# Performance work log

Measured on AMD Instinct MI355X. Metric: run time of the kernel, lower is better.

Reference implementation:

```python
import jax, jax.numpy as jnp
import numpy as np

B, T, D = 4, 2048, 2048
H = 16
NOPE, ROPE, VD = 64, 64, 128
QK = NOPE + ROPE  # 128
KV_R, Q_R = 512, 1024
EPS = 1e-6
THETA = 10000.0
SCALE = 1.0 / np.sqrt(QK)


def rmsnorm(x, g):
    var = jnp.mean(jnp.square(x), axis=-1, keepdims=True)
    return x * jax.lax.rsqrt(var + EPS) * g


def rope_tables(seq_len, dim):
    inv_freq = 1.0 / (THETA ** (np.arange(0, dim, 2, dtype=np.float32) / dim))
    t = np.arange(seq_len, dtype=np.float32)
    freqs = np.outer(t, inv_freq)              # [T, dim/2]
    emb = np.concatenate([freqs, freqs], -1)   # [T, dim]
    return jnp.asarray(np.cos(emb)), jnp.asarray(np.sin(emb))


def rotate_half(x):
    x1, x2 = jnp.split(x, 2, axis=-1)
    return jnp.concatenate([-x2, x1], axis=-1)


def apply_rope(x, cos, sin):
    # x: [B,H,S,dim]; cos/sin: [S,dim] -> broadcast over B,H
    return x * cos[None, None] + rotate_half(x) * sin[None, None]


def setup_inputs() -> dict:
    key = jax.random.key(0)
    ks = jax.random.split(key, 10)
    w = lambda k, shp: jax.random.normal(k, shp, jnp.float32) * 0.02
    return {
        'x': jax.random.normal(ks[0], (B, T, D), jnp.float32),
        'w_q_down': w(ks[1], (D, Q_R)),
        'g_q_down': jnp.ones((Q_R,), jnp.float32),
        'w_q_up': w(ks[2], (Q_R, H * QK)),
        'w_kv_down': w(ks[3], (D, KV_R)),
        'g_kv_down': jnp.ones((KV_R,), jnp.float32),
        'w_k_up': w(ks[4], (KV_R, H * NOPE)),
        'w_v_up': w(ks[5], (KV_R, H * VD)),
        'w_k_rope': w(ks[6], (D, ROPE)),
        'g_q': jnp.ones((QK,), jnp.float32),
        'g_k': jnp.ones((QK,), jnp.float32),
        'w_gate': w(ks[7], (D, H * VD)),
        'w_o': w(ks[8], (H * VD, D)),
    }


def reference(x, w_q_down, g_q_down, w_q_up, w_kv_down, g_kv_down,
              w_k_up, w_v_up, w_k_rope, g_q, g_k, w_gate, w_o):
    cos, sin = rope_tables(T, ROPE)

    # Low-rank Q: down-proj -> RMSNorm -> up-proj
    q_c = rmsnorm(x @ w_q_down, g_q_down)                       # [B,T,Q_R]
    q = (q_c @ w_q_up).reshape(B, T, H, QK).transpose(0, 2, 1, 3)  # [B,H,T,QK]
    q_nope, q_rope = q[..., :NOPE], q[..., NOPE:]

    # Low-rank KV compression
    c_kv = rmsnorm(x @ w_kv_down, g_kv_down)                    # [B,S,KV_R]
    k_rope = x @ w_k_rope                                       # [B,S,ROPE]
    S = T
    k_nope = (c_kv @ w_k_up).reshape(B, S, H, NOPE).transpose(0, 2, 1, 3)
    v = (c_kv @ w_v_up).reshape(B, S, H, VD).transpose(0, 2, 1, 3)

    # Decoupled RoPE: shared k_rope broadcast over heads
    k_rope = jnp.broadcast_to(k_rope[:, None], (B, H, S, ROPE))
    q_rope = apply_rope(q_rope, cos[:T], sin[:T])
    k_rope = apply_rope(k_rope, cos[:S], sin[:S])

    q = rmsnorm(jnp.concatenate([q_nope, q_rope], -1), g_q)     # [B,H,T,QK]
    k = rmsnorm(jnp.concatenate([k_nope, k_rope], -1), g_k)     # [B,H,S,QK]

    # Causal SDPA
    scores = jnp.einsum('bhtd,bhsd->bhts', q, k) * SCALE
    mask = jnp.tril(jnp.ones((T, S), bool))
    scores = jnp.where(mask, scores, jnp.finfo(scores.dtype).min)
    attn = jax.nn.softmax(scores, axis=-1)
    out = jnp.einsum('bhts,bhsd->bhtd', attn, v)                # [B,H,T,VD]

    # Gating
    gate = (x @ w_gate).reshape(B, T, H, VD).transpose(0, 2, 1, 3)
    out = out * jax.nn.silu(gate)

    out = out.transpose(0, 2, 1, 3).reshape(B, T, H * VD)
    return out @ w_o
```

## Files before the change

### kernel.cpp

```cpp
#include <hip/hip_runtime.h>
#include <hip/hip_bf16.h>
#include <math.h>

typedef __bf16 bf16_t;
typedef __bf16 bf16x4 __attribute__((ext_vector_type(4)));
typedef __bf16 bf16x8 __attribute__((ext_vector_type(8)));
typedef float f32x4 __attribute__((ext_vector_type(4)));

#define SCALE_F 0.08838834764831845f
#define SMAX_F 14.0f

#define GLOAD_LDS16(gp, lp)                                              \
    __builtin_amdgcn_global_load_lds(                                    \
        (const __attribute__((address_space(1))) void*)(gp),             \
        (__attribute__((address_space(3))) void*)(lp), 16, 0, 0)

__global__ void k_convert(const float* __restrict__ in, bf16_t* __restrict__ out, int n) {
    int i = (blockIdx.x * 256 + threadIdx.x) * 4;
    if (i >= n) return;
    float4 f = *(const float4*)(in + i);
    out[i + 0] = (bf16_t)f.x;
    out[i + 1] = (bf16_t)f.y;
    out[i + 2] = (bf16_t)f.z;
    out[i + 3] = (bf16_t)f.w;
}

__global__ void k_transpose(const float* __restrict__ w, bf16_t* __restrict__ wt, int K, int N) {
    __shared__ float tile[32][33];
    int n0 = blockIdx.x * 32, k0 = blockIdx.y * 32;
    int tx = threadIdx.x & 31, ty = threadIdx.x >> 5;
#pragma unroll
    for (int i = 0; i < 32; i += 8)
        tile[ty + i][tx] = w[(size_t)(k0 + ty + i) * N + (n0 + tx)];
    __syncthreads();
#pragma unroll
    for (int i = 0; i < 32; i += 8)
        wt[(size_t)(n0 + ty + i) * K + (k0 + tx)] = (bf16_t)tile[tx][ty + i];
}

__global__ void k_rope_tables(float* __restrict__ cosT, float* __restrict__ sinT) {
    int idx = blockIdx.x * 256 + threadIdx.x;
    int t = idx >> 6, i = idx & 63;
    float invf = powf(10000.f, -(float)(i & 31) / 32.f);
    float ang = (float)t * invf;
    float s, c;
    sincosf(ang, &s, &c);
    cosT[idx] = c;
    sinT[idx] = s;
}

__global__ void k_rmsnorm(bf16_t* __restrict__ x, const float* __restrict__ g, int C) {
    bf16_t* p = x + (size_t)blockIdx.x * C;
    float ss = 0.f;
    for (int i = threadIdx.x; i < C; i += 256) {
        float v = (float)p[i];
        ss += v * v;
    }
#pragma unroll
    for (int m = 32; m; m >>= 1) ss += __shfl_xor(ss, m);
    __shared__ float red[4];
    if ((threadIdx.x & 63) == 0) red[threadIdx.x >> 6] = ss;
    __syncthreads();
    float tot = red[0] + red[1] + red[2] + red[3];
    float scale = rsqrtf(tot / (float)C + 1e-6f);
    for (int i = threadIdx.x; i < C; i += 256)
        p[i] = (bf16_t)((float)p[i] * scale * g[i]);
}

template <int OUTF32>
__global__ __launch_bounds__(256) void k_gemm(const bf16_t* __restrict__ A,
                                              const bf16_t* __restrict__ Bt,
                                              void* __restrict__ Cp, int M, int N, int K,
                                              size_t sA, size_t sB, size_t sC) {
    __shared__ bf16_t As[2][128 * 32];
    __shared__ bf16_t Bs[2][128 * 32];
    A += (size_t)blockIdx.z * sA;
    Bt += (size_t)blockIdx.z * sB;
    const size_t coff = (size_t)blockIdx.z * sC;
    const int bm = blockIdx.y * 128, bn = blockIdx.x * 128;
    const int tid = threadIdx.x, lane = tid & 63, wv = tid >> 6;
    const int quad = lane >> 4, l16 = lane & 15;
    const int wm = (wv >> 1) * 64, wn = (wv & 1) * 64;
    f32x4 acc[4][4] = {};
    const int sr0 = wv * 32 + (lane >> 2);
    const int scc = (lane & 3) * 8;
    const int lo0 = (wv * 2) * 512, lo1 = (wv * 2 + 1) * 512;
    const bool bok0 = (bn + sr0) < N;
    const bool bok1 = (bn + sr0 + 16) < N;
    for (int k0 = 0; k0 < K; k0 += 64) {
        const bf16_t* gA = A + (size_t)(bm + sr0) * K + k0 + scc;
        const bf16_t* gB = Bt + (size_t)(bn + sr0) * K + k0 + scc;
        GLOAD_LDS16(gA, As[0] + lo0);
        GLOAD_LDS16(gA + (size_t)16 * K, As[0] + lo1);
        GLOAD_LDS16(gA + 32, As[1] + lo0);
        GLOAD_LDS16(gA + (size_t)16 * K + 32, As[1] + lo1);
        if (bok0) {
            GLOAD_LDS16(gB, Bs[0] + lo0);
            GLOAD_LDS16(gB + 32, Bs[1] + lo0);
        }
        if (bok1) {
            GLOAD_LDS16(gB + (size_t)16 * K, Bs[0] + lo1);
            GLOAD_LDS16(gB + (size_t)16 * K + 32, Bs[1] + lo1);
        }
        __syncthreads();
#pragma unroll
        for (int hf = 0; hf < 2; ++hf) {
            bf16x8 af[4], bfr[4];
#pragma unroll
            for (int mi = 0; mi < 4; ++mi)
                af[mi] = *(bf16x8*)(As[hf] + (wm + mi * 16 + l16) * 32 + quad * 8);
#pragma unroll
            for (int ni = 0; ni < 4; ++ni)
                bfr[ni] = *(bf16x8*)(Bs[hf] + (wn + ni * 16 + l16) * 32 + quad * 8);
#pragma unroll
            for (int mi = 0; mi < 4; ++mi)
#pragma unroll
                for (int ni = 0; ni < 4; ++ni)
                    acc[mi][ni] = __builtin_amdgcn_mfma_f32_16x16x32_bf16(af[mi], bfr[ni],
                                                                          acc[mi][ni], 0, 0, 0);
        }
        __syncthreads();
    }
#pragma unroll
    for (int mi = 0; mi < 4; ++mi)
#pragma unroll
        for (int ni = 0; ni < 4; ++ni)
#pragma unroll
            for (int r = 0; r < 4; ++r) {
                int row = bm + wm + mi * 16 + quad * 4 + r;
                int col = bn + wn + ni * 16 + l16;
                if (col < N) {
                    if constexpr (OUTF32)
                        ((float*)Cp)[coff + (size_t)row * N + col] = acc[mi][ni][r];
                    else
                        ((bf16_t*)Cp)[coff + (size_t)row * N + col] = (bf16_t)acc[mi][ni][r];
                }
            }
}

__global__ void k_build_q(bf16_t* __restrict__ q, const float* __restrict__ g,
                          const float* __restrict__ cosT, const float* __restrict__ sinT) {
    int wid = blockIdx.x * 4 + (threadIdx.x >> 6);
    int lane = threadIdx.x & 63;
    int row = wid >> 4, h = wid & 15;
    int t = row & 2047;
    bf16_t* p = q + (size_t)row * 2048 + h * 128;
    float x0 = (float)p[lane];
    float x1 = (float)p[64 + lane];
    float xp = (float)p[64 + (lane ^ 32)];
    float c = cosT[t * 64 + lane], s = sinT[t * 64 + lane];
    float rot = (lane < 32) ? -xp : xp;
    float y1 = x1 * c + rot * s;
    float ss = x0 * x0 + y1 * y1;
#pragma unroll
    for (int m = 32; m; m >>= 1) ss += __shfl_xor(ss, m);
    float scale = rsqrtf(ss / 128.f + 1e-6f);
    p[lane] = (bf16_t)(x0 * scale * g[lane]);
    p[64 + lane] = (bf16_t)(y1 * scale * g[64 + lane]);
}

__global__ void k_build_k(const bf16_t* __restrict__ knope, const bf16_t* __restrict__ krope,
                          bf16_t* __restrict__ kout, const float* __restrict__ g,
                          const float* __restrict__ cosT, const float* __restrict__ sinT) {
    int wid = blockIdx.x * 4 + (threadIdx.x >> 6);
    int lane = threadIdx.x & 63;
    int row = wid >> 4, h = wid & 15;
    int t = row & 2047;
    float x0 = (float)knope[(size_t)row * 1024 + h * 64 + lane];
    float x1 = (float)krope[(size_t)row * 64 + lane];
    float xp = (float)krope[(size_t)row * 64 + (lane ^ 32)];
    float c = cosT[t * 64 + lane], s = sinT[t * 64 + lane];
    float rot = (lane < 32) ? -xp : xp;
    float y1 = x1 * c + rot * s;
    float ss = x0 * x0 + y1 * y1;
#pragma unroll
    for (int m = 32; m; m >>= 1) ss += __shfl_xor(ss, m);
    float scale = rsqrtf(ss / 128.f + 1e-6f);
    bf16_t* p = kout + (size_t)row * 2048 + h * 128;
    p[lane] = (bf16_t)(x0 * scale * g[lane]);
    p[64 + lane] = (bf16_t)(y1 * scale * g[64 + lane]);
}

__global__ __launch_bounds__(512, 4) void k_attn(const bf16_t* __restrict__ q,
                                                 const bf16_t* __restrict__ k,
                                                 const bf16_t* __restrict__ vT,
                                                 const bf16_t* __restrict__ gate,
                                                 bf16_t* __restrict__ o) {
    __shared__ bf16_t Ks[64 * 136];
    __shared__ bf16_t Vt[128 * 72];
    __shared__ float lbuf[128];
    const int qb = (int)gridDim.x - 1 - (int)blockIdx.x;
    const int bh = blockIdx.y;
    const int b = bh >> 4, h = bh & 15;
    const int t0 = qb * 128;
    const int tid = threadIdx.x, lane = tid & 63, wv = tid >> 6;
    const int quad = lane >> 4, l16 = lane & 15;
    const int wrow = t0 + wv * 16;

    bf16x8 aq[4];
    {
        const bf16_t* qp = q + ((size_t)(b * 2048 + wrow + l16)) * 2048 + h * 128 + quad * 8;
#pragma unroll
        for (int kk = 0; kk < 4; ++kk) aq[kk] = *(const bf16x8*)(qp + kk * 32);
    }
    f32x4 oacc[8] = {};
    float l_lane = 0.f;

    const bf16_t* vbase = vT + ((size_t)b * 2048 + (size_t)h * 128) * 2048;
    const bf16_t* kbase = k + ((size_t)b * 2048) * 2048 + h * 128;

    const int krow = tid >> 4;
    const int kcol = (tid & 15) * 8;
    const int kds = krow * 136 + kcol;
    const int vrow = tid >> 3;
    const int vcol = (tid & 7) * 8;
    const int a8 = tid & 7;
    const int pb0 = (a8 >> 2) * 32 + (a8 & 1) * 16 + ((a8 >> 1) & 1) * 4;
    const int vds = vrow * 72 + pb0;

    const int nkb = 2 * qb + 2;
    bf16x8 kreg0, kreg1, vreg0, vreg1;
    {
        kreg0 = *(const bf16x8*)(kbase + (size_t)krow * 2048 + kcol);
        kreg1 = *(const bf16x8*)(kbase + (size_t)(krow + 32) * 2048 + kcol);
        vreg0 = *(const bf16x8*)(vbase + (size_t)vrow * 2048 + vcol);
        vreg1 = *(const bf16x8*)(vbase + (size_t)(vrow + 64) * 2048 + vcol);
    }
    for (int kb = 0; kb < nkb; ++kb) {
        const int s0 = kb * 64;
        __syncthreads();
        *(bf16x8*)(Ks + kds) = kreg0;
        *(bf16x8*)(Ks + kds + 32 * 136) = kreg1;
        {
            bf16x4 v0lo = __builtin_shufflevector(vreg0, vreg0, 0, 1, 2, 3);
            bf16x4 v0hi = __builtin_shufflevector(vreg0, vreg0, 4, 5, 6, 7);
            bf16x4 v1lo = __builtin_shufflevector(vreg1, vreg1, 0, 1, 2, 3);
            bf16x4 v1hi = __builtin_shufflevector(vreg1, vreg1, 4, 5, 6, 7);
            *(bf16x4*)(Vt + vds) = v0lo;
            *(bf16x4*)(Vt + vds + 8) = v0hi;
            *(bf16x4*)(Vt + vds + 64 * 72) = v1lo;
            *(bf16x4*)(Vt + vds + 64 * 72 + 8) = v1hi;
        }
        __syncthreads();
        if (kb + 1 < nkb) {
            const int sn = s0 + 64;
            kreg0 = *(const bf16x8*)(kbase + (size_t)(sn + krow) * 2048 + kcol);
            kreg1 = *(const bf16x8*)(kbase + (size_t)(sn + krow + 32) * 2048 + kcol);
            vreg0 = *(const bf16x8*)(vbase + (size_t)vrow * 2048 + sn + vcol);
            vreg1 = *(const bf16x8*)(vbase + (size_t)(vrow + 64) * 2048 + sn + vcol);
        }
        if (s0 > wrow + 15) continue;
        f32x4 sc[4] = {};
#pragma unroll
        for (int ni = 0; ni < 4; ++ni)
#pragma unroll
            for (int kk = 0; kk < 4; ++kk) {
                bf16x8 ak = *(bf16x8*)(Ks + (ni * 16 + l16) * 136 + kk * 32 + quad * 8);
                sc[ni] = __builtin_amdgcn_mfma_f32_16x16x32_bf16(ak, aq[kk], sc[ni], 0, 0, 0);
            }
        const int tq = wrow + l16;
#pragma unroll
        for (int ni = 0; ni < 4; ++ni) {
            const int sb = s0 + ni * 16 + quad * 4;
#pragma unroll
            for (int r2 = 0; r2 < 4; ++r2) {
                float pv = __expf(sc[ni][r2] * SCALE_F - SMAX_F);
                if (sb + r2 > tq) pv = 0.f;
                sc[ni][r2] = pv;
                l_lane += pv;
            }
        }
        bf16x8 pa0, pa1;
#pragma unroll
        for (int r2 = 0; r2 < 4; ++r2) {
            pa0[r2] = (bf16_t)sc[0][r2];
            pa0[4 + r2] = (bf16_t)sc[1][r2];
            pa1[r2] = (bf16_t)sc[2][r2];
            pa1[4 + r2] = (bf16_t)sc[3][r2];
        }
#pragma unroll
        for (int nd = 0; nd < 8; ++nd) {
            bf16x8 bv = *(bf16x8*)(Vt + (nd * 16 + l16) * 72 + quad * 8);
            oacc[nd] = __builtin_amdgcn_mfma_f32_16x16x32_bf16(pa0, bv, oacc[nd], 0, 0, 0);
        }
#pragma unroll
        for (int nd = 0; nd < 8; ++nd) {
            bf16x8 bv = *(bf16x8*)(Vt + (nd * 16 + l16) * 72 + 32 + quad * 8);
            oacc[nd] = __builtin_amdgcn_mfma_f32_16x16x32_bf16(pa1, bv, oacc[nd], 0, 0, 0);
        }
    }
    l_lane += __shfl_xor(l_lane, 16);
    l_lane += __shfl_xor(l_lane, 32);
    if (quad == 0) lbuf[wv * 16 + l16] = l_lane;
    float rl[4];
#pragma unroll
    for (int r2 = 0; r2 < 4; ++r2) rl[r2] = 1.f / lbuf[wv * 16 + quad * 4 + r2];
#pragma unroll
    for (int nd = 0; nd < 8; ++nd) {
        int d = nd * 16 + l16;
#pragma unroll
        for (int r2 = 0; r2 < 4; ++r2) {
            int trow = wrow + quad * 4 + r2;
            size_t gi = ((size_t)(b * 2048 + trow)) * 2048 + h * 128 + d;
            float gt = (float)gate[gi];
            float sg = gt / (1.f + __expf(-gt));
            o[gi] = (bf16_t)((oacc[nd][r2] * rl[r2]) * sg);
        }
    }
}

extern "C" void kernel_launch(void* const* d_in, const int* in_sizes, int n_in,
                              void* d_out, int out_size, void* d_ws, size_t ws_size,
                              hipStream_t stream) {
    const float* x         = (const float*)d_in[0];
    const float* w_q_down  = (const float*)d_in[1];
    const float* g_q_down  = (const float*)d_in[2];
    const float* w_q_up    = (const float*)d_in[3];
    const float* w_kv_down = (const float*)d_in[4];
    const float* g_kv_down = (const float*)d_in[5];
    const float* w_k_up    = (const float*)d_in[6];
    const float* w_v_up    = (const float*)d_in[7];
    const float* w_k_rope  = (const float*)d_in[8];
    const float* g_q       = (const float*)d_in[9];
    const float* g_k       = (const float*)d_in[10];
    const float* w_gate    = (const float*)d_in[11];
    const float* w_o       = (const float*)d_in[12];
    float* out = (float*)d_out;

    char* base = (char*)d_ws;
    size_t off = 0;
    auto alloc = [&](size_t bytes) -> void* {
        void* p = base + off;
        off = (off + bytes + 255) & ~(size_t)255;
        return p;
    };
    const size_t MT = 8192;
    bf16_t* xb     = (bf16_t*)alloc(MT * 2048 * 2);
    bf16_t* wqd_t  = (bf16_t*)alloc((size_t)1024 * 2048 * 2);
    bf16_t* wqu_t  = (bf16_t*)alloc((size_t)2048 * 1024 * 2);
    bf16_t* wkvd_t = (bf16_t*)alloc((size_t)512 * 2048 * 2);
    bf16_t* wku_t  = (bf16_t*)alloc((size_t)1024 * 512 * 2);
    bf16_t* wvu_t  = (bf16_t*)alloc((size_t)2048 * 512 * 2);
    bf16_t* wkr_t  = (bf16_t*)alloc((size_t)64 * 2048 * 2);
    bf16_t* wg_t   = (bf16_t*)alloc((size_t)2048 * 2048 * 2);
    bf16_t* wo_t   = (bf16_t*)alloc((size_t)2048 * 2048 * 2);
    bf16_t* qc     = (bf16_t*)alloc(MT * 1024 * 2);
    bf16_t* ckv    = (bf16_t*)alloc(MT * 512 * 2);
    bf16_t* krope  = (bf16_t*)alloc(MT * 64 * 2);
    bf16_t* vT     = (bf16_t*)alloc(MT * 2048 * 2);
    bf16_t* gbuf   = (bf16_t*)alloc(MT * 2048 * 2);
    float* cosT    = (float*)alloc((size_t)2048 * 64 * 4);
    float* sinT    = (float*)alloc((size_t)2048 * 64 * 4);
    bf16_t* knope = qc;
    bf16_t* qbuf  = (bf16_t*)d_out;
    bf16_t* kbuf  = (bf16_t*)d_out + MT * 2048;
    bf16_t* obuf  = xb;

    k_convert<<<dim3(16384), dim3(256), 0, stream>>>(x, xb, 16777216);
    k_transpose<<<dim3(32, 64), 256, 0, stream>>>(w_q_down, wqd_t, 2048, 1024);
    k_transpose<<<dim3(64, 32), 256, 0, stream>>>(w_q_up, wqu_t, 1024, 2048);
    k_transpose<<<dim3(16, 64), 256, 0, stream>>>(w_kv_down, wkvd_t, 2048, 512);
    k_transpose<<<dim3(32, 16), 256, 0, stream>>>(w_k_up, wku_t, 512, 1024);
    k_transpose<<<dim3(64, 16), 256, 0, stream>>>(w_v_up, wvu_t, 512, 2048);
    k_transpose<<<dim3(2, 64), 256, 0, stream>>>(w_k_rope, wkr_t, 2048, 64);
    k_transpose<<<dim3(64, 64), 256, 0, stream>>>(w_gate, wg_t, 2048, 2048);
    k_transpose<<<dim3(64, 64), 256, 0, stream>>>(w_o, wo_t, 2048, 2048);
    k_rope_tables<<<dim3(512), 256, 0, stream>>>(cosT, sinT);
    k_gemm<0><<<dim3(8, 64), 256, 0, stream>>>(xb, wqd_t, qc, 8192, 1024, 2048, 0, 0, 0);
    k_rmsnorm<<<dim3(8192), 256, 0, stream>>>(qc, g_q_down, 1024);
    k_gemm<0><<<dim3(16, 64), 256, 0, stream>>>(qc, wqu_t, qbuf, 8192, 2048, 1024, 0, 0, 0);
    k_gemm<0><<<dim3(4, 64), 256, 0, stream>>>(xb, wkvd_t, ckv, 8192, 512, 2048, 0, 0, 0);
    k_rmsnorm<<<dim3(8192), 256, 0, stream>>>(ckv, g_kv_down, 512);
    k_gemm<0><<<dim3(8, 64), 256, 0, stream>>>(ckv, wku_t, knope, 8192, 1024, 512, 0, 0, 0);
    k_gemm<0><<<dim3(16, 16, 4), 256, 0, stream>>>(wvu_t, ckv, vT, 2048, 2048, 512,
                                                   0, (size_t)2048 * 512, (size_t)2048 * 2048);
    k_gemm<0><<<dim3(1, 64), 256, 0, stream>>>(xb, wkr_t, krope, 8192, 64, 2048, 0, 0, 0);
    k_gemm<0><<<dim3(16, 64), 256, 0, stream>>>(xb, wg_t, gbuf, 8192, 2048, 2048, 0, 0, 0);
    k_build_q<<<dim3(32768), 256, 0, stream>>>(qbuf, g_q, cosT, sinT);
    k_build_k<<<dim3(32768), 256, 0, stream>>>(knope, krope, kbuf, g_k, cosT, sinT);
    k_attn<<<dim3(16, 64), 512, 0, stream>>>(qbuf, kbuf, vT, gbuf, obuf);
    k_gemm<1><<<dim3(16, 64), 256, 0, stream>>>(obuf, wo_t, out, 8192, 2048, 2048, 0, 0, 0);
}
```

Baseline: 766.9 us.

## Give each attention wave two 16-row query tiles to reuse K/V LDS reads

Result: slower. 793.1 us (+3.4%).

```diff
diff --git a/kernel.cpp b/kernel.cpp
--- a/kernel.cpp
+++ b/kernel.cpp
@@ -181,7 +181,7 @@
     p[64 + lane] = (bf16_t)(y1 * scale * g[64 + lane]);
 }
 
-__global__ __launch_bounds__(512, 4) void k_attn(const bf16_t* __restrict__ q,
+__global__ __launch_bounds__(256, 2) void k_attn(const bf16_t* __restrict__ q,
                                                  const bf16_t* __restrict__ k,
                                                  const bf16_t* __restrict__ vT,
                                                  const bf16_t* __restrict__ gate,
@@ -195,16 +195,18 @@
     const int t0 = qb * 128;
     const int tid = threadIdx.x, lane = tid & 63, wv = tid >> 6;
     const int quad = lane >> 4, l16 = lane & 15;
-    const int wrow = t0 + wv * 16;
-
-    bf16x8 aq[4];
-    {
-        const bf16_t* qp = q + ((size_t)(b * 2048 + wrow + l16)) * 2048 + h * 128 + quad * 8;
-#pragma unroll
-        for (int kk = 0; kk < 4; ++kk) aq[kk] = *(const bf16x8*)(qp + kk * 32);
-    }
-    f32x4 oacc[8] = {};
-    float l_lane = 0.f;
+    const int wrow = t0 + wv * 32;
+
+    bf16x8 aq[2][4];
+#pragma unroll
+    for (int mi = 0; mi < 2; ++mi) {
+        const bf16_t* qp =
+            q + ((size_t)(b * 2048 + wrow + mi * 16 + l16)) * 2048 + h * 128 + quad * 8;
+#pragma unroll
+        for (int kk = 0; kk < 4; ++kk) aq[mi][kk] = *(const bf16x8*)(qp + kk * 32);
+    }
+    f32x4 oacc[2][8] = {};
+    float l_lane[2] = {0.f, 0.f};
 
     const bf16_t* vbase = vT + ((size_t)b * 2048 + (size_t)h * 128) * 2048;
     const bf16_t* kbase = k + ((size_t)b * 2048) * 2048 + h * 128;
@@ -212,101 +214,112 @@
     const int krow = tid >> 4;
     const int kcol = (tid & 15) * 8;
     const int kds = krow * 136 + kcol;
-    const int vrow = tid >> 3;
-    const int vcol = (tid & 7) * 8;
-    const int a8 = tid & 7;
-    const int pb0 = (a8 >> 2) * 32 + (a8 & 1) * 16 + ((a8 >> 1) & 1) * 4;
-    const int vds = vrow * 72 + pb0;
+    const int vrow = tid >> 1;
+    const int vkk = tid & 1;
+    const int vds = vrow * 72 + vkk * 32;
 
     const int nkb = 2 * qb + 2;
-    bf16x8 kreg0, kreg1, vreg0, vreg1;
+    bf16x8 kreg[4], vreg[4];
     {
-        kreg0 = *(const bf16x8*)(kbase + (size_t)krow * 2048 + kcol);
-        kreg1 = *(const bf16x8*)(kbase + (size_t)(krow + 32) * 2048 + kcol);
-        vreg0 = *(const bf16x8*)(vbase + (size_t)vrow * 2048 + vcol);
-        vreg1 = *(const bf16x8*)(vbase + (size_t)(vrow + 64) * 2048 + vcol);
+#pragma unroll
+        for (int i = 0; i < 4; ++i)
+            kreg[i] = *(const bf16x8*)(kbase + (size_t)(krow + 16 * i) * 2048 + kcol);
+#pragma unroll
+        for (int j = 0; j < 4; ++j)
+            vreg[j] = *(const bf16x8*)(vbase + (size_t)vrow * 2048 + vkk * 32 + j * 8);
     }
     for (int kb = 0; kb < nkb; ++kb) {
         const int s0 = kb * 64;
         __syncthreads();
-        *(bf16x8*)(Ks + kds) = kreg0;
-        *(bf16x8*)(Ks + kds + 32 * 136) = kreg1;
+#pragma unroll
+        for (int i = 0; i < 4; ++i) *(bf16x8*)(Ks + kds + i * (16 * 136)) = kreg[i];
         {
-            bf16x4 v0lo = __builtin_shufflevector(vreg0, vreg0, 0, 1, 2, 3);
-            bf16x4 v0hi = __builtin_shufflevector(vreg0, vreg0, 4, 5, 6, 7);
-            bf16x4 v1lo = __builtin_shufflevector(vreg1, vreg1, 0, 1, 2, 3);
-            bf16x4 v1hi = __builtin_shufflevector(vreg1, vreg1, 4, 5, 6, 7);
-            *(bf16x4*)(Vt + vds) = v0lo;
-            *(bf16x4*)(Vt + vds + 8) = v0hi;
-            *(bf16x4*)(Vt + vds + 64 * 72) = v1lo;
-            *(bf16x4*)(Vt + vds + 64 * 72 + 8) = v1hi;
+            bf16x8 o0 = __builtin_shufflevector(vreg[0], vreg[2], 0, 1, 2, 3, 8, 9, 10, 11);
+            bf16x8 o1 = __builtin_shufflevector(vreg[0], vreg[2], 4, 5, 6, 7, 12, 13, 14, 15);
+            bf16x8 o2 = __builtin_shufflevector(vreg[1], vreg[3], 0, 1, 2, 3, 8, 9, 10, 11);
+            bf16x8 o3 = __builtin_shufflevector(vreg[1], vreg[3], 4, 5, 6, 7, 12, 13, 14, 15);
+            *(bf16x8*)(Vt + vds) = o0;
+            *(bf16x8*)(Vt + vds + 8) = o1;
+            *(bf16x8*)(Vt + vds + 16) = o2;
+            *(bf16x8*)(Vt + vds + 24) = o3;
         }
         __syncthreads();
         if (kb + 1 < nkb) {
             const int sn = s0 + 64;
-            kreg0 = *(const bf16x8*)(kbase + (size_t)(sn + krow) * 2048 + kcol);
-            kreg1 = *(const bf16x8*)(kbase + (size_t)(sn + krow + 32) * 2048 + kcol);
-            vreg0 = *(const bf16x8*)(vbase + (size_t)vrow * 2048 + sn + vcol);
-            vreg1 = *(const bf16x8*)(vbase + (size_t)(vrow + 64) * 2048 + sn + vcol);
-        }
-        if (s0 > wrow + 15) continue;
-        f32x4 sc[4] = {};
-#pragma unroll
-        for (int ni = 0; ni < 4; ++ni)
+#pragma unroll
+            for (int i = 0; i < 4; ++i)
+                kreg[i] = *(const bf16x8*)(kbase + (size_t)(sn + krow + 16 * i) * 2048 + kcol);
+#pragma unroll
+            for (int j = 0; j < 4; ++j)
+                vreg[j] = *(const bf16x8*)(vbase + (size_t)vrow * 2048 + sn + vkk * 32 + j * 8);
+        }
+        if (s0 > wrow + 31) continue;
+        const int tq0 = wrow + l16;
+        const int tq1 = wrow + 16 + l16;
+        bf16x8 pa[2][2];
+#pragma unroll
+        for (int ni = 0; ni < 4; ++ni) {
+            f32x4 sc0 = {0.f, 0.f, 0.f, 0.f};
+            f32x4 sc1 = {0.f, 0.f, 0.f, 0.f};
 #pragma unroll
             for (int kk = 0; kk < 4; ++kk) {
                 bf16x8 ak = *(bf16x8*)(Ks + (ni * 16 + l16) * 136 + kk * 32 + quad * 8);
-                sc[ni] = __builtin_amdgcn_mfma_f32_16x16x32_bf16(ak, aq[kk], sc[ni], 0, 0, 0);
-            }
-        const int tq = wrow + l16;
-#pragma unroll
-        for (int ni = 0; ni < 4; ++ni) {
+                sc0 = __builtin_amdgcn_mfma_f32_16x16x32_bf16(ak, aq[0][kk], sc0, 0, 0, 0);
+                sc1 = __builtin_amdgcn_mfma_f32_16x16x32_bf16(ak, aq[1][kk], sc1, 0, 0, 0);
+            }
             const int sb = s0 + ni * 16 + quad * 4;
 #pragma unroll
             for (int r2 = 0; r2 < 4; ++r2) {
-                float pv = __expf(sc[ni][r2] * SCALE_F - SMAX_F);
-                if (sb + r2 > tq) pv = 0.f;
-                sc[ni][r2] = pv;
-                l_lane += pv;
-            }
-        }
-        bf16x8 pa0, pa1;
-#pragma unroll
-        for (int r2 = 0; r2 < 4; ++r2) {
-            pa0[r2] = (bf16_t)sc[0][r2];
-            pa0[4 + r2] = (bf16_t)sc[1][r2];
-            pa1[r2] = (bf16_t)sc[2][r2];
-            pa1[4 + r2] = (bf16_t)sc[3][r2];
-        }
+                float pv0 = __expf(sc0[r2] * SCALE_F - SMAX_F);
+                float pv1 = __expf(sc1[r2] * SCALE_F - SMAX_F);
+                if (sb + r2 > tq0) pv0 = 0.f;
+                if (sb + r2 > tq1) pv1 = 0.f;
+                l_lane[0] += pv0;
+                l_lane[1] += pv1;
+                pa[0][ni >> 1][(ni & 1) * 4 + r2] = (bf16_t)pv0;
+                pa[1][ni >> 1][(ni & 1) * 4 + r2] = (bf16_t)pv1;
+            }
+        }
+#pragma unroll
+        for (int kh = 0; kh < 2; ++kh)
+#pragma unroll
+            for (int nd = 0; nd < 8; ++nd) {
+                bf16x8 bv = *(bf16x8*)(Vt + (nd * 16 + l16) * 72 + kh * 32 + quad * 8);
+                oacc[0][nd] =
+                    __builtin_amdgcn_mfma_f32_16x16x32_bf16(pa[0][kh], bv, oacc[0][nd], 0, 0, 0);
+                oacc[1][nd] =
+                    __builtin_amdgcn_mfma_f32_16x16x32_bf16(pa[1][kh], bv, oacc[1][nd], 0, 0, 0);
+            }
+    }
+#pragma unroll
+    for (int mi = 0; mi < 2; ++mi) {
+        l_lane[mi] += __shfl_xor(l_lane[mi], 16);
+        l_lane[mi] += __shfl_xor(l_lane[mi], 32);
+    }
+    if (quad == 0) {
+        lbuf[wv * 32 + l16] = l_lane[0];
+        lbuf[wv * 32 + 16 + l16] = l_lane[1];
+    }
+    float rl[2][4];
+#pragma unroll
+    for (int mi = 0; mi < 2; ++mi)
+#pragma unroll
+        for (int r2 = 0; r2 < 4; ++r2)
+            rl[mi][r2] = 1.f / lbuf[wv * 32 + mi * 16 + quad * 4 + r2];
+#pragma unroll
+    for (int mi = 0; mi < 2; ++mi)
 #pragma unroll
         for (int nd = 0; nd < 8; ++nd) {
-            bf16x8 bv = *(bf16x8*)(Vt + (nd * 16 + l16) * 72 + quad * 8);
-            oacc[nd] = __builtin_amdgcn_mfma_f32_16x16x32_bf16(pa0, bv, oacc[nd], 0, 0, 0);
-        }
-#pragma unroll
-        for (int nd = 0; nd < 8; ++nd) {
-            bf16x8 bv = *(bf16x8*)(Vt + (nd * 16 + l16) * 72 + 32 + quad * 8);
-            oacc[nd] = __builtin_amdgcn_mfma_f32_16x16x32_bf16(pa1, bv, oacc[nd], 0, 0, 0);
-        }
-    }
-    l_lane += __shfl_xor(l_lane, 16);
-    l_lane += __shfl_xor(l_lane, 32);
-    if (quad == 0) lbuf[wv * 16 + l16] = l_lane;
-    float rl[4];
-#pragma unroll
-    for (int r2 = 0; r2 < 4; ++r2) rl[r2] = 1.f / lbuf[wv * 16 + quad * 4 + r2];
-#pragma unroll
-    for (int nd = 0; nd < 8; ++nd) {
-        int d = nd * 16 + l16;
-#pragma unroll
-        for (int r2 = 0; r2 < 4; ++r2) {
-            int trow = wrow + quad * 4 + r2;
-            size_t gi = ((size_t)(b * 2048 + trow)) * 2048 + h * 128 + d;
-            float gt = (float)gate[gi];
-            float sg = gt / (1.f + __expf(-gt));
-            o[gi] = (bf16_t)((oacc[nd][r2] * rl[r2]) * sg);
-        }
-    }
+            int d = nd * 16 + l16;
+#pragma unroll
+            for (int r2 = 0; r2 < 4; ++r2) {
+                int trow = wrow + mi * 16 + quad * 4 + r2;
+                size_t gi = ((size_t)(b * 2048 + trow)) * 2048 + h * 128 + d;
+                float gt = (float)gate[gi];
+                float sg = gt / (1.f + __expf(-gt));
+                o[gi] = (bf16_t)((oacc[mi][nd][r2] * rl[mi][r2]) * sg);
+            }
+        }
 }
 
 extern "C" void kernel_launch(void* const* d_in, const int* in_sizes, int n_in,
@@ -378,6 +391,6 @@
     k_gemm<0><<<dim3(16, 64), 256, 0, stream>>>(xb, wg_t, gbuf, 8192, 2048, 2048, 0, 0, 0);
     k_build_q<<<dim3(32768), 256, 0, stream>>>(qbuf, g_q, cosT, sinT);
     k_build_k<<<dim3(32768), 256, 0, stream>>>(knope, krope, kbuf, g_k, cosT, sinT);
-    k_attn<<<dim3(16, 64), 512, 0, stream>>>(qbuf, kbuf, vT, gbuf, obuf);
+    k_attn<<<dim3(16, 64), 256, 0, stream>>>(qbuf, kbuf, vT, gbuf, obuf);
     k_gemm<1><<<dim3(16, 64), 256, 0, stream>>>(obuf, wo_t, out, 8192, 2048, 2048, 0, 0, 0);
 }
```
